# Optimization experiments

Hardware: AMD Instinct MI355X
Metric: run time of the kernel (lower is better)

## Reference

```python
import jax, jax.numpy as jnp
import numpy as np


def setup_inputs() -> dict:
    key = jax.random.key(0)
    k1, k2, k3, k4 = jax.random.split(key, 4)
    Q = jax.random.normal(k1, (32, 32, 128), dtype=jnp.float32)
    D = jax.random.normal(k2, (512, 180, 128), dtype=jnp.float32)
    q_mask = jax.random.randint(k3, (32, 32), 0, 2, dtype=jnp.int32)
    d_mask = jax.random.randint(k4, (512, 180), 0, 2, dtype=jnp.int32)
    return {"Q": Q, "D": D, "q_mask": q_mask, "d_mask": d_mask}


def reference(Q, D, q_mask, d_mask):
    # ColBERT MaxSim late-interaction scoring (ColBERT_List_qa.score)
    # Q: [q, m, h], D: [d, n, h]; masks zero out padding token embeddings.
    Qm = Q * q_mask.astype(Q.dtype)[..., None]              # [q, m, h]
    Dm = D * d_mask.astype(D.dtype)[..., None]              # [d, n, h]
    sim = jnp.einsum("qmh,dnh->qdmn", Qm, Dm)               # [q, d, m, n]
    scores = sim.max(axis=-1).sum(axis=-1)                  # max over doc tokens n, sum over query tokens m -> [q, d]
    return scores
```

## Files before the change

### kernel.cpp

```cpp
#include <hip/hip_runtime.h>
#include <hip/hip_bf16.h>

typedef __attribute__((ext_vector_type(8))) short short8;
typedef __attribute__((ext_vector_type(4))) float f32x4;

#define NQ 32
#define NM 32
#define NH 128
#define ND 512
#define NN 180
#define NTMAX 12
#define MTILES 64
#define LSTR 136

#define QFRAG_BYTES (MTILES * 4 * 64 * 16)
#define QSTART_OFF  QFRAG_BYTES
#define T2_OFF      (QSTART_OFF + 33 * 4)

static __device__ __forceinline__ unsigned short f2bf(float x) {
  __hip_bfloat16 h = __float2bfloat16(x);
  return __builtin_bit_cast(unsigned short, h);
}

static __device__ __forceinline__ uint4 pack8(float4 a, float4 b) {
  unsigned int x = (unsigned)f2bf(a.x) | ((unsigned)f2bf(a.y) << 16);
  unsigned int y = (unsigned)f2bf(a.z) | ((unsigned)f2bf(a.w) << 16);
  unsigned int z = (unsigned)f2bf(b.x) | ((unsigned)f2bf(b.y) << 16);
  unsigned int u = (unsigned)f2bf(b.z) | ((unsigned)f2bf(b.w) << 16);
  return make_uint4(x, y, z, u);
}

__global__ __launch_bounds__(256) void prep_q_compact(
    const float* __restrict__ Q, const int* __restrict__ qmask,
    unsigned short* __restrict__ Qb, int* __restrict__ qstart_g,
    int* __restrict__ t2_g) {
  __shared__ unsigned short src_tok[NQ * NM];
  __shared__ int rtot[16];
  const int tid = threadIdx.x;
  const int lane = tid & 63;
  const int wv = tid >> 6;

  int flags[4], pres[4];
  #pragma unroll
  for (int r = 0; r < 4; ++r) {
    int idx = r * 256 + tid;
    int f = qmask[idx];
    unsigned long long bal = __ballot(f != 0);
    int pre = __popcll(bal & ((1ull << lane) - 1ull));
    if (lane == 63) rtot[r * 4 + wv] = pre + (f ? 1 : 0);
    flags[r] = f;
    pres[r] = pre;
  }
  __syncthreads();
  int total = 0;
  int chunkbase[4];
  {
    int run = 0;
    #pragma unroll
    for (int r = 0; r < 4; ++r) {
      chunkbase[r] = run + ((wv >= 1) ? rtot[r * 4 + 0] : 0) +
                           ((wv >= 2) ? rtot[r * 4 + 1] : 0) +
                           ((wv >= 3) ? rtot[r * 4 + 2] : 0);
      run += rtot[r * 4 + 0] + rtot[r * 4 + 1] + rtot[r * 4 + 2] + rtot[r * 4 + 3];
    }
    total = run;
  }
  #pragma unroll
  for (int r = 0; r < 4; ++r) {
    int idx = r * 256 + tid;
    int pos = chunkbase[r] + pres[r];
    if (flags[r]) src_tok[pos] = (unsigned short)idx;
    if (blockIdx.x == 0 && (idx & 31) == 0) qstart_g[idx >> 5] = pos;
  }
  __syncthreads();
  if (blockIdx.x == 0 && tid == 0) {
    qstart_g[32] = total;
    int T = (total + 15) >> 4;
    t2_g[0] = (T + 1) >> 1;
  }

  {
    int s = blockIdx.x * 256 + tid;
    int t2 = s >> 8, ks = (s >> 6) & 3, ln = s & 63;
    int col = t2 * 16 + (ln & 15);
    int kk = ks * 32 + (ln >> 4) * 8;
    uint4 o = make_uint4(0u, 0u, 0u, 0u);
    if (col < total) {
      int tok = src_tok[col];
      const float* src = Q + tok * NH + kk;
      float4 a = *reinterpret_cast<const float4*>(src);
      float4 b = *reinterpret_cast<const float4*>(src + 4);
      o = pack8(a, b);
    }
    reinterpret_cast<uint4*>(Qb)[s] = o;
  }
}

__global__ __launch_bounds__(512, 4) void fused_maxsim(
    const float* __restrict__ D, const int* __restrict__ dmask,
    const unsigned short* __restrict__ Qb, const int* __restrict__ qstart_g,
    const int* __restrict__ t2_g, float* __restrict__ out) {
  __shared__ unsigned short Dlds[192 * LSTR];
  __shared__ float colmax[MTILES * 16];
  __shared__ unsigned short mapinv[192];
  __shared__ int wtot[4];
  const int d = blockIdx.x;
  const int tid = threadIdx.x;
  const int lane = tid & 63;
  const int w = tid >> 6;
  const float NEG = -__builtin_inff();

  int flag = 0, pre = 0;
  if (tid < NN) flag = dmask[d * NN + tid];
  if (tid < 192) {
    unsigned long long bal = __ballot(flag != 0);
    pre = __popcll(bal & ((1ull << lane) - 1ull));
    if (lane == 63) wtot[w] = pre + (flag ? 1 : 0);
  }
  __syncthreads();
  const int cnt = wtot[0] + wtot[1] + wtot[2];
  if (tid < 192 && flag) {
    int base = (w >= 1 ? wtot[0] : 0) + (w >= 2 ? wtot[1] : 0);
    mapinv[pre + base] = (unsigned short)tid;
  }
  __syncthreads();

  const int T2 = t2_g[0];

  short8 Qp0[4], Qp1[4];
  const bool hasFirst = (w < T2);
  {
    const int t0 = w * 2;
    #pragma unroll
    for (int ks = 0; ks < 4; ++ks) {
      Qp0[ks] = *reinterpret_cast<const short8*>(
          reinterpret_cast<const char*>(Qb) +
          (((t0 * 4 + ks) << 10) + (lane << 4)));
      Qp1[ks] = *reinterpret_cast<const short8*>(
          reinterpret_cast<const char*>(Qb) +
          ((((t0 + 1) * 4 + ks) << 10) + (lane << 4)));
    }
  }

  const int ntc = (cnt + 15) >> 4;
  {
    const int rg = tid >> 5;
    const int c4 = tid & 31;
    const int nrows = ntc * 16;
    #pragma unroll 4
    for (int base = 0; base < nrows; base += 16) {
      int dr = base + rg;
      uint2 o = make_uint2(0u, 0u);
      if (dr < cnt) {
        int sr = mapinv[dr];
        float4 v = reinterpret_cast<const float4*>(D)[(size_t)(d * NN + sr) * 32 + c4];
        o.x = (unsigned)f2bf(v.x) | ((unsigned)f2bf(v.y) << 16);
        o.y = (unsigned)f2bf(v.z) | ((unsigned)f2bf(v.w) << 16);
      }
      *reinterpret_cast<uint2*>(&Dlds[dr * LSTR + c4 * 4]) = o;
    }
  }
  __syncthreads();

  const int bl = lane & 15;
  const int bg = lane >> 4;

  #pragma unroll 1
  for (int tp = w; tp < T2; tp += 8) {
    const int t0 = tp * 2;

    short8 Qf0[4], Qf1[4];
    if (tp == w) {
      #pragma unroll
      for (int ks = 0; ks < 4; ++ks) { Qf0[ks] = Qp0[ks]; Qf1[ks] = Qp1[ks]; }
    } else {
      #pragma unroll
      for (int ks = 0; ks < 4; ++ks) {
        Qf0[ks] = *reinterpret_cast<const short8*>(
            reinterpret_cast<const char*>(Qb) +
            (((t0 * 4 + ks) << 10) + (lane << 4)));
        Qf1[ks] = *reinterpret_cast<const short8*>(
            reinterpret_cast<const char*>(Qb) +
            ((((t0 + 1) * 4 + ks) << 10) + (lane << 4)));
      }
    }

    float run0 = NEG, run1 = NEG;

    #pragma unroll 2
    for (int nt = 0; nt < ntc; ++nt) {
      short8 Da[4];
      #pragma unroll
      for (int ks = 0; ks < 4; ++ks)
        Da[ks] = *reinterpret_cast<const short8*>(
            &Dlds[(nt * 16 + bl) * LSTR + ks * 32 + bg * 8]);

      f32x4 acc0 = {0.f, 0.f, 0.f, 0.f};
      f32x4 acc1 = acc0;
      #pragma unroll
      for (int ks = 0; ks < 4; ++ks) {
        acc0 = __builtin_amdgcn_mfma_f32_16x16x32_bf16(Da[ks], Qf0[ks], acc0, 0, 0, 0);
        acc1 = __builtin_amdgcn_mfma_f32_16x16x32_bf16(Da[ks], Qf1[ks], acc1, 0, 0, 0);
      }

      if (nt * 16 + 16 > cnt) {
        const int rlim = cnt - nt * 16 - bg * 4;
        float v0 = NEG, v1 = NEG;
        #pragma unroll
        for (int j = 0; j < 4; ++j) {
          v0 = fmaxf(v0, (j < rlim) ? acc0[j] : NEG);
          v1 = fmaxf(v1, (j < rlim) ? acc1[j] : NEG);
        }
        run0 = fmaxf(run0, v0);
        run1 = fmaxf(run1, v1);
      } else {
        run0 = fmaxf(run0, fmaxf(fmaxf(acc0[0], acc0[1]), fmaxf(acc0[2], acc0[3])));
        run1 = fmaxf(run1, fmaxf(fmaxf(acc1[0], acc1[1]), fmaxf(acc1[2], acc1[3])));
      }
    }

    if (cnt < NN) {
      run0 = fmaxf(run0, 0.f);
      run1 = fmaxf(run1, 0.f);
    }

    run0 = fmaxf(run0, __shfl_xor(run0, 16));
    run0 = fmaxf(run0, __shfl_xor(run0, 32));
    run1 = fmaxf(run1, __shfl_xor(run1, 16));
    run1 = fmaxf(run1, __shfl_xor(run1, 32));

    if (lane < 16) {
      colmax[t0 * 16 + lane] = run0;
      colmax[(t0 + 1) * 16 + lane] = run1;
    }
  }
  __syncthreads();

  if (tid < NQ) {
    const int s0 = qstart_g[tid];
    const int s1 = qstart_g[tid + 1];
    float s = 0.f;
    for (int i = s0; i < s1; ++i) s += colmax[i];
    out[tid * ND + d] = s;
  }
}

extern "C" void kernel_launch(void* const* d_in, const int* in_sizes, int n_in,
                              void* d_out, int out_size, void* d_ws, size_t ws_size,
                              hipStream_t stream) {
  const float* Q = (const float*)d_in[0];
  const float* D = (const float*)d_in[1];
  const int* qmask = (const int*)d_in[2];
  const int* dmask = (const int*)d_in[3];
  float* out = (float*)d_out;

  unsigned short* Qb = (unsigned short*)d_ws;
  int* qstart_g = (int*)((char*)d_ws + QSTART_OFF);
  int* t2_g = (int*)((char*)d_ws + T2_OFF);

  prep_q_compact<<<64, 256, 0, stream>>>(Q, qmask, Qb, qstart_g, t2_g);
  fused_maxsim<<<ND, 512, 0, stream>>>(D, dmask, Qb, qstart_g, t2_g, out);
}
```

Before: 21.61 us.

## Fuse query compaction and bf16 conversion into the main MaxSim kernel

Removes the separate prep kernel. Every block now compacts the query mask itself into shared memory, then gathers and converts the Q rows to bf16 straight from the fp32 input. This drops one kernel launch and the dependency between the two kernels. In exchange, all 512 blocks repeat the mask scan and read fp32 Q (twice the bytes, gathered by token), which adds per-block work and global traffic.

```diff
diff --git a/kernel.cpp b/kernel.cpp
--- a/kernel.cpp
+++ b/kernel.cpp
@@ -9,13 +9,8 @@
 #define NH 128
 #define ND 512
 #define NN 180
-#define NTMAX 12
 #define MTILES 64
 #define LSTR 136
-
-#define QFRAG_BYTES (MTILES * 4 * 64 * 16)
-#define QSTART_OFF  QFRAG_BYTES
-#define T2_OFF      (QSTART_OFF + 33 * 4)
 
 static __device__ __forceinline__ unsigned short f2bf(float x) {
   __hip_bfloat16 h = __float2bfloat16(x);
@@ -30,119 +25,100 @@
   return make_uint4(x, y, z, u);
 }
 
-__global__ __launch_bounds__(256) void prep_q_compact(
-    const float* __restrict__ Q, const int* __restrict__ qmask,
-    unsigned short* __restrict__ Qb, int* __restrict__ qstart_g,
-    int* __restrict__ t2_g) {
-  __shared__ unsigned short src_tok[NQ * NM];
-  __shared__ int rtot[16];
-  const int tid = threadIdx.x;
-  const int lane = tid & 63;
-  const int wv = tid >> 6;
-
-  int flags[4], pres[4];
-  #pragma unroll
-  for (int r = 0; r < 4; ++r) {
-    int idx = r * 256 + tid;
-    int f = qmask[idx];
-    unsigned long long bal = __ballot(f != 0);
-    int pre = __popcll(bal & ((1ull << lane) - 1ull));
-    if (lane == 63) rtot[r * 4 + wv] = pre + (f ? 1 : 0);
-    flags[r] = f;
-    pres[r] = pre;
-  }
-  __syncthreads();
-  int total = 0;
-  int chunkbase[4];
-  {
-    int run = 0;
-    #pragma unroll
-    for (int r = 0; r < 4; ++r) {
-      chunkbase[r] = run + ((wv >= 1) ? rtot[r * 4 + 0] : 0) +
-                           ((wv >= 2) ? rtot[r * 4 + 1] : 0) +
-                           ((wv >= 3) ? rtot[r * 4 + 2] : 0);
-      run += rtot[r * 4 + 0] + rtot[r * 4 + 1] + rtot[r * 4 + 2] + rtot[r * 4 + 3];
-    }
-    total = run;
-  }
-  #pragma unroll
-  for (int r = 0; r < 4; ++r) {
-    int idx = r * 256 + tid;
-    int pos = chunkbase[r] + pres[r];
-    if (flags[r]) src_tok[pos] = (unsigned short)idx;
-    if (blockIdx.x == 0 && (idx & 31) == 0) qstart_g[idx >> 5] = pos;
-  }
-  __syncthreads();
-  if (blockIdx.x == 0 && tid == 0) {
-    qstart_g[32] = total;
-    int T = (total + 15) >> 4;
-    t2_g[0] = (T + 1) >> 1;
-  }
-
-  {
-    int s = blockIdx.x * 256 + tid;
-    int t2 = s >> 8, ks = (s >> 6) & 3, ln = s & 63;
-    int col = t2 * 16 + (ln & 15);
-    int kk = ks * 32 + (ln >> 4) * 8;
-    uint4 o = make_uint4(0u, 0u, 0u, 0u);
-    if (col < total) {
-      int tok = src_tok[col];
-      const float* src = Q + tok * NH + kk;
-      float4 a = *reinterpret_cast<const float4*>(src);
-      float4 b = *reinterpret_cast<const float4*>(src + 4);
-      o = pack8(a, b);
-    }
-    reinterpret_cast<uint4*>(Qb)[s] = o;
-  }
-}
-
 __global__ __launch_bounds__(512, 4) void fused_maxsim(
-    const float* __restrict__ D, const int* __restrict__ dmask,
-    const unsigned short* __restrict__ Qb, const int* __restrict__ qstart_g,
-    const int* __restrict__ t2_g, float* __restrict__ out) {
+    const float* __restrict__ Q, const float* __restrict__ D,
+    const int* __restrict__ qmask, const int* __restrict__ dmask,
+    float* __restrict__ out) {
   __shared__ unsigned short Dlds[192 * LSTR];
   __shared__ float colmax[MTILES * 16];
   __shared__ unsigned short mapinv[192];
+  __shared__ unsigned short src_tok[1040];
+  __shared__ int qstart_s[33];
   __shared__ int wtot[4];
+  __shared__ int rtot[16];
   const int d = blockIdx.x;
   const int tid = threadIdx.x;
   const int lane = tid & 63;
   const int w = tid >> 6;
   const float NEG = -__builtin_inff();
 
-  int flag = 0, pre = 0;
-  if (tid < NN) flag = dmask[d * NN + tid];
+  int dflag = 0, dpre = 0;
+  if (tid < NN) dflag = dmask[d * NN + tid];
   if (tid < 192) {
-    unsigned long long bal = __ballot(flag != 0);
-    pre = __popcll(bal & ((1ull << lane) - 1ull));
-    if (lane == 63) wtot[w] = pre + (flag ? 1 : 0);
-  }
-  __syncthreads();
+    unsigned long long bal = __ballot(dflag != 0);
+    dpre = __popcll(bal & ((1ull << lane) - 1ull));
+    if (lane == 63) wtot[w] = dpre + (dflag ? 1 : 0);
+  }
+  int qflags[2], qpres[2];
+  #pragma unroll
+  for (int r = 0; r < 2; ++r) {
+    int f = qmask[r * 512 + tid];
+    unsigned long long bal = __ballot(f != 0);
+    int pre = __popcll(bal & ((1ull << lane) - 1ull));
+    if (lane == 63) rtot[r * 8 + w] = pre + (f ? 1 : 0);
+    qflags[r] = f;
+    qpres[r] = pre;
+  }
+  src_tok[tid] = 0;
+  src_tok[tid + 512] = 0;
+  if (tid < 16) src_tok[1024 + tid] = 0;
+  __syncthreads();
+
   const int cnt = wtot[0] + wtot[1] + wtot[2];
-  if (tid < 192 && flag) {
+  if (tid < 192 && dflag) {
     int base = (w >= 1 ? wtot[0] : 0) + (w >= 2 ? wtot[1] : 0);
-    mapinv[pre + base] = (unsigned short)tid;
-  }
-  __syncthreads();
-
-  const int T2 = t2_g[0];
+    mapinv[dpre + base] = (unsigned short)tid;
+  }
+  int total, chunkbase[2];
+  {
+    int run = 0;
+    #pragma unroll
+    for (int r = 0; r < 2; ++r) {
+      int cb = run;
+      #pragma unroll
+      for (int i = 0; i < 8; ++i) {
+        if (i < w) cb += rtot[r * 8 + i];
+        run += rtot[r * 8 + i];
+      }
+      chunkbase[r] = cb;
+    }
+    total = run;
+  }
+  #pragma unroll
+  for (int r = 0; r < 2; ++r) {
+    int idx = r * 512 + tid;
+    int pos = chunkbase[r] + qpres[r];
+    if (qflags[r]) src_tok[pos] = (unsigned short)idx;
+    if ((idx & 31) == 0) qstart_s[idx >> 5] = pos;
+  }
+  if (tid == 0) qstart_s[32] = total;
+  const int T = (total + 15) >> 4;
+  const int T2 = (T + 1) >> 1;
+  __syncthreads();
+
+  const int bl = lane & 15;
+  const int bg = lane >> 4;
+  const int ntc = (cnt + 15) >> 4;
 
   short8 Qp0[4], Qp1[4];
-  const bool hasFirst = (w < T2);
   {
     const int t0 = w * 2;
+    const int tokA = src_tok[t0 * 16 + bl];
+    const int tokB = src_tok[t0 * 16 + 16 + bl];
+    const float* qA = Q + tokA * NH + bg * 8;
+    const float* qB = Q + tokB * NH + bg * 8;
     #pragma unroll
     for (int ks = 0; ks < 4; ++ks) {
-      Qp0[ks] = *reinterpret_cast<const short8*>(
-          reinterpret_cast<const char*>(Qb) +
-          (((t0 * 4 + ks) << 10) + (lane << 4)));
-      Qp1[ks] = *reinterpret_cast<const short8*>(
-          reinterpret_cast<const char*>(Qb) +
-          ((((t0 + 1) * 4 + ks) << 10) + (lane << 4)));
-    }
-  }
-
-  const int ntc = (cnt + 15) >> 4;
+      float4 a0 = *reinterpret_cast<const float4*>(qA + ks * 32);
+      float4 a1 = *reinterpret_cast<const float4*>(qA + ks * 32 + 4);
+      float4 b0 = *reinterpret_cast<const float4*>(qB + ks * 32);
+      float4 b1 = *reinterpret_cast<const float4*>(qB + ks * 32 + 4);
+      Qp0[ks] = __builtin_bit_cast(short8, pack8(a0, a1));
+      Qp1[ks] = __builtin_bit_cast(short8, pack8(b0, b1));
+      asm volatile("" : "+v"(Qp0[ks]), "+v"(Qp1[ks]));
+    }
+  }
+
   {
     const int rg = tid >> 5;
     const int c4 = tid & 31;
@@ -162,9 +138,6 @@
   }
   __syncthreads();
 
-  const int bl = lane & 15;
-  const int bg = lane >> 4;
-
   #pragma unroll 1
   for (int tp = w; tp < T2; tp += 8) {
     const int t0 = tp * 2;
@@ -174,14 +147,19 @@
       #pragma unroll
       for (int ks = 0; ks < 4; ++ks) { Qf0[ks] = Qp0[ks]; Qf1[ks] = Qp1[ks]; }
     } else {
+      const int tokA = src_tok[t0 * 16 + bl];
+      const int tokB = src_tok[t0 * 16 + 16 + bl];
+      const float* qA = Q + tokA * NH + bg * 8;
+      const float* qB = Q + tokB * NH + bg * 8;
       #pragma unroll
       for (int ks = 0; ks < 4; ++ks) {
-        Qf0[ks] = *reinterpret_cast<const short8*>(
-            reinterpret_cast<const char*>(Qb) +
-            (((t0 * 4 + ks) << 10) + (lane << 4)));
-        Qf1[ks] = *reinterpret_cast<const short8*>(
-            reinterpret_cast<const char*>(Qb) +
-            ((((t0 + 1) * 4 + ks) << 10) + (lane << 4)));
+        float4 a0 = *reinterpret_cast<const float4*>(qA + ks * 32);
+        float4 a1 = *reinterpret_cast<const float4*>(qA + ks * 32 + 4);
+        float4 b0 = *reinterpret_cast<const float4*>(qB + ks * 32);
+        float4 b1 = *reinterpret_cast<const float4*>(qB + ks * 32 + 4);
+        Qf0[ks] = __builtin_bit_cast(short8, pack8(a0, a1));
+        Qf1[ks] = __builtin_bit_cast(short8, pack8(b0, b1));
+        asm volatile("" : "+v"(Qf0[ks]), "+v"(Qf1[ks]));
       }
     }
 
@@ -237,8 +215,8 @@
   __syncthreads();
 
   if (tid < NQ) {
-    const int s0 = qstart_g[tid];
-    const int s1 = qstart_g[tid + 1];
+    const int s0 = qstart_s[tid];
+    const int s1 = qstart_s[tid + 1];
     float s = 0.f;
     for (int i = s0; i < s1; ++i) s += colmax[i];
     out[tid * ND + d] = s;
@@ -254,10 +232,5 @@
   const int* dmask = (const int*)d_in[3];
   float* out = (float*)d_out;
 
-  unsigned short* Qb = (unsigned short*)d_ws;
-  int* qstart_g = (int*)((char*)d_ws + QSTART_OFF);
-  int* t2_g = (int*)((char*)d_ws + T2_OFF);
-
-  prep_q_compact<<<64, 256, 0, stream>>>(Q, qmask, Qb, qstart_g, t2_g);
-  fused_maxsim<<<ND, 512, 0, stream>>>(D, dmask, Qb, qstart_g, t2_g, out);
-}
+  fused_maxsim<<<ND, 512, 0, stream>>>(Q, D, qmask, dmask, out);
+}
```

New measurement: 27.68 us. 1.28x slower.
